# Optimization experiments

Hardware: AMD Instinct MI355X
Metric: run time of the kernel (lower is better)

## Reference

```python
import jax, jax.numpy as jnp
import numpy as np

D, H, HD, F, L, V, R = 4096, 32, 128, 11008, 2, 32002, 64
ALPHA = 16.0
B, S = 2, 1024
EPS = 1e-5


def setup_inputs() -> dict:
    key = jax.random.key(0)
    ks = jax.random.split(key, 24)
    n = lambda k, shape: (jax.random.normal(k, shape, jnp.float32) * 0.02)
    return {
        "input_ids": jax.random.randint(ks[0], (B, S), 0, V),
        "attention_mask": jnp.ones((B, S), jnp.int32),
        "embed": n(ks[1], (V, D)),
        "Wq": n(ks[2], (L, D, D)), "Wk": n(ks[3], (L, D, D)),
        "Wv": n(ks[4], (L, D, D)), "Wo": n(ks[5], (L, D, D)),
        "Aq": n(ks[6], (L, R, D)), "Bq": jnp.zeros((L, D, R), jnp.float32),
        "Ak": n(ks[7], (L, R, D)), "Bk": n(ks[8], (L, D, R)),
        "Av": n(ks[9], (L, R, D)), "Bv": n(ks[10], (L, D, R)),
        "Ao": n(ks[11], (L, R, D)), "Bo": n(ks[12], (L, D, R)),
        "Wgate": n(ks[13], (L, F, D)), "Wup": n(ks[14], (L, F, D)),
        "Wdown": n(ks[15], (L, D, F)),
        "attn_norm_w": jnp.ones((L, D), jnp.float32),
        "mlp_norm_w": jnp.ones((L, D), jnp.float32),
        "final_norm_w": jnp.ones((D,), jnp.float32),
        "cls_W": n(ks[16], (3, D)), "cls_b": jnp.zeros((3,), jnp.float32),
    }


def _rmsnorm(x, w):
    var = jnp.mean(jnp.square(x), axis=-1, keepdims=True)
    return (x * jax.lax.rsqrt(var + EPS)) * w


def _rope(seq_len):
    inv = 1.0 / (10000.0 ** (jnp.arange(0, HD, 2, dtype=jnp.float32) / HD))
    freqs = jnp.outer(jnp.arange(seq_len, dtype=jnp.float32), inv)  # [S, HD/2]
    emb = jnp.concatenate([freqs, freqs], -1)  # [S, HD]
    return jnp.cos(emb), jnp.sin(emb)


def _rot_half(x):
    h = x.shape[-1] // 2
    return jnp.concatenate([-x[..., h:], x[..., :h]], -1)


def _lora(h, W, A, Bm):
    # h @ W.T + (alpha/r) * (h @ A.T) @ B.T   (dropout inactive in eval)
    return h @ W.T + (h @ A.T) @ Bm.T * (ALPHA / R)


def reference(input_ids, attention_mask, embed, Wq, Wk, Wv, Wo,
              Aq, Bq, Ak, Bk, Av, Bv, Ao, Bo,
              Wgate, Wup, Wdown, attn_norm_w, mlp_norm_w, final_norm_w,
              cls_W, cls_b):
    b, s = input_ids.shape
    x = embed[input_ids]  # [B,S,D]
    cos, sin = _rope(s)  # [S,HD]
    causal = jnp.tril(jnp.ones((s, s), bool))
    mask = causal[None, None] & (attention_mask[:, None, None, :] > 0)
    bias = jnp.where(mask, 0.0, -1e9).astype(jnp.float32)  # [B,1,S,S]

    def heads(t):  # [B,S,D] -> [B,H,S,HD]
        return t.reshape(b, s, H, HD).transpose(0, 2, 1, 3)

    for l in range(L):
        h = _rmsnorm(x, attn_norm_w[l])
        q = heads(_lora(h, Wq[l], Aq[l], Bq[l]))
        k = heads(_lora(h, Wk[l], Ak[l], Bk[l]))
        v = heads(_lora(h, Wv[l], Av[l], Bv[l]))
        q = q * cos + _rot_half(q) * sin
        k = k * cos + _rot_half(k) * sin
        scores = jnp.einsum('bhqd,bhkd->bhqk', q, k) / np.sqrt(HD) + bias
        attn = jax.nn.softmax(scores, axis=-1)
        o = jnp.einsum('bhqk,bhkd->bhqd', attn, v)
        o = o.transpose(0, 2, 1, 3).reshape(b, s, D)
        x = x + _lora(o, Wo[l], Ao[l], Bo[l])
        h = _rmsnorm(x, mlp_norm_w[l])
        x = x + (jax.nn.silu(h @ Wgate[l].T) * (h @ Wup[l].T)) @ Wdown[l].T

    x = _rmsnorm(x, final_norm_w)
    cls = x[:, 0, :]  # [CLS] at position 0 (right padding)
    return cls @ cls_W.T + cls_b
```

## Files before the change

### kernel.cpp

```cpp
#include <hip/hip_runtime.h>
#include <cstdint>
#include <cstddef>

#define D_   4096
#define H_   32
#define HD_  128
#define F_   11008
#define L_   2
#define R_   64
#define BB   2
#define SS   1024
#define TOK  (BB*SS)
#define N3   12288
#define EPS_ 1e-5f

typedef __attribute__((ext_vector_type(8))) short          s16x8;
typedef __attribute__((ext_vector_type(4))) float          fx4;
typedef __attribute__((ext_vector_type(4))) unsigned short u16x4t;
typedef __attribute__((ext_vector_type(8))) unsigned short u16x8t;

__device__ __forceinline__ unsigned short f2bf(float f) {
  union { float f; unsigned u; } x; x.f = f;
  unsigned r = (x.u + 0x7FFFu + ((x.u >> 16) & 1u)) >> 16;
  return (unsigned short)r;
}
__device__ __forceinline__ float b2f(unsigned short h) {
  union { unsigned u; float f; } x; x.u = ((unsigned)h) << 16;
  return x.f;
}

__device__ __forceinline__ void xcd_remap(int nwg, int mt_cnt, int& mt, int& nt) {
  const int orig = blockIdx.x;
  const int q = nwg >> 3, r = nwg & 7;
  const int xcd = orig & 7, i = orig >> 3;
  const int wgid = (xcd < r ? xcd * (q + 1) : r * (q + 1) + (xcd - r) * q) + i;
  mt = wgid % mt_cnt;
  nt = wgid / mt_cnt;
}

__global__ void k_embed(const int* __restrict__ ids, const float* __restrict__ emb,
                        float* __restrict__ x) {
  const int tok = blockIdx.x, tid = threadIdx.x;
  const int id = ids[tok];
  const float* s = emb + (size_t)id * D_;
  float* d = x + (size_t)tok * D_;
#pragma unroll
  for (int i = 0; i < 4; ++i)
    *(fx4*)(d + i * 1024 + tid * 4) = *(const fx4*)(s + i * 1024 + tid * 4);
}

__global__ __launch_bounds__(256) void k_cvt(const float* __restrict__ src,
                                             unsigned short* __restrict__ dst, int n) {
  const int stride = gridDim.x * 256 * 8;
  for (int i = (blockIdx.x * 256 + threadIdx.x) * 8; i < n; i += stride) {
    fx4 a = *(const fx4*)(src + i);
    fx4 b = *(const fx4*)(src + i + 4);
    u16x8t p;
    p[0] = f2bf(a[0]); p[1] = f2bf(a[1]); p[2] = f2bf(a[2]); p[3] = f2bf(a[3]);
    p[4] = f2bf(b[0]); p[5] = f2bf(b[1]); p[6] = f2bf(b[2]); p[7] = f2bf(b[3]);
    *(u16x8t*)(dst + i) = p;
  }
}

__global__ __launch_bounds__(256) void k_rmsnorm(const float* __restrict__ x,
                                                 const float* __restrict__ w,
                                                 unsigned short* __restrict__ out) {
  const int row = blockIdx.x, tid = threadIdx.x;
  const float* xr = x + (size_t)row * D_;
  fx4 v[4];
  float ss = 0.f;
#pragma unroll
  for (int i = 0; i < 4; ++i) {
    v[i] = *(const fx4*)(xr + i * 1024 + tid * 4);
    ss += v[i][0]*v[i][0] + v[i][1]*v[i][1] + v[i][2]*v[i][2] + v[i][3]*v[i][3];
  }
#pragma unroll
  for (int off = 32; off > 0; off >>= 1) ss += __shfl_down(ss, off);
  __shared__ float red[4];
  if ((tid & 63) == 0) red[tid >> 6] = ss;
  __syncthreads();
  const float sc = rsqrtf((red[0] + red[1] + red[2] + red[3]) * (1.f / D_) + EPS_);
  unsigned short* orow = out + (size_t)row * D_;
#pragma unroll
  for (int i = 0; i < 4; ++i) {
    fx4 wv = *(const fx4*)(w + i * 1024 + tid * 4);
    u16x4t pk;
    pk.x = f2bf(v[i][0] * sc * wv[0]);
    pk.y = f2bf(v[i][1] * sc * wv[1]);
    pk.z = f2bf(v[i][2] * sc * wv[2]);
    pk.w = f2bf(v[i][3] * sc * wv[3]);
    *(u16x4t*)(orow + i * 1024 + tid * 4) = pk;
  }
}

template <int NFRAG>
__global__ __launch_bounds__(256, 2) void k_lmid(const unsigned short* __restrict__ Ain,
                                                 const float* __restrict__ P0,
                                                 const float* __restrict__ P1,
                                                 const float* __restrict__ P2,
                                                 float* __restrict__ part) {
  __shared__ unsigned short sA[64 * 64];
  __shared__ unsigned short sW[NFRAG * 16 * 72];
  const int tid = threadIdx.x, wave = tid >> 6, lane = tid & 63;
  const int l15 = lane & 15, l4 = lane >> 4;
  const int m0 = blockIdx.x * 64;
  const int kbase = blockIdx.y * 512;
  const int arow = tid >> 3;
  const int acol = (((tid & 7) ^ (arow & 7)) << 3);
  const int brow = tid >> 4;
  const int bcol = (tid & 15) << 2;
  const float* ptrs[3] = {P0, P1, P2};

  fx4 acc[NFRAG];
#pragma unroll
  for (int j = 0; j < NFRAG; ++j) acc[j] = (fx4){0.f, 0.f, 0.f, 0.f};

  for (int t = 0; t < 8; ++t) {
    const int kb = kbase + t * 64;
#pragma unroll
    for (int i = 0; i < 2; ++i) {
      const unsigned short* gp = Ain + (size_t)(m0 + i * 32 + arow) * 4096 + kb + acol;
      unsigned short* lp = sA + i * 2048 + wave * 512;
      __builtin_amdgcn_global_load_lds(
          (const __attribute__((address_space(1))) unsigned int*)gp,
          (__attribute__((address_space(3))) unsigned int*)lp, 16, 0, 0);
    }
#pragma unroll
    for (int j = 0; j < NFRAG; ++j) {
      const float* wp = ptrs[j >> 2] + (size_t)((j & 3) * 16 + brow) * 4096 + kb + bcol;
      fx4 v = *(const fx4*)wp;
      u16x4t pk;
      pk.x = f2bf(v[0]); pk.y = f2bf(v[1]); pk.z = f2bf(v[2]); pk.w = f2bf(v[3]);
      *(u16x4t*)&sW[(j * 16 + brow) * 72 + bcol] = pk;
    }
    __syncthreads();
#pragma unroll
    for (int ks = 0; ks < 2; ++ks) {
      const int row = wave * 16 + l15;
      const int cid = (((ks * 4) + l4) ^ (row & 7)) << 3;
      s16x8 af = *(const s16x8*)&sA[row * 64 + cid];
#pragma unroll
      for (int j = 0; j < NFRAG; ++j) {
        s16x8 bf = *(const s16x8*)&sW[(j * 16 + l15) * 72 + ks * 32 + (l4 << 3)];
        acc[j] = __builtin_amdgcn_mfma_f32_16x16x32_bf16(af, bf, acc[j], 0, 0, 0);
      }
    }
    __syncthreads();
  }
  const size_t base = (size_t)blockIdx.y * 2048 * (NFRAG * 16);
#pragma unroll
  for (int j = 0; j < NFRAG; ++j)
#pragma unroll
    for (int r = 0; r < 4; ++r)
      part[base + (size_t)(m0 + wave * 16 + l4 * 4 + r) * (NFRAG * 16) + j * 16 + l15] = acc[j][r];
}

__global__ void k_lmred(const float* __restrict__ part, unsigned short* __restrict__ outb, int ld) {
  const int idx = blockIdx.x * 256 + threadIdx.x;
  const int stride = 2048 * ld;
  float s = 0.f;
#pragma unroll
  for (int ks = 0; ks < 8; ++ks) s += part[(size_t)ks * stride + idx];
  outb[idx] = f2bf(0.25f * s);
}

template <int EPI, bool EXT>
__global__ __launch_bounds__(256, 4) void k_gemm(const unsigned short* __restrict__ A,
                                                 const unsigned short* __restrict__ Wb,
                                                 float* __restrict__ outF,
                                                 unsigned short* __restrict__ outB,
                                                 const float* __restrict__ auxF,
                                                 const unsigned short* __restrict__ Aext,
                                                 int ldaE,
                                                 const unsigned short* __restrict__ Wext,
                                                 int M, int N, int K, int nwg) {
  __shared__ unsigned short sA[128 * 64];
  __shared__ unsigned short sB[128 * 64];
  const int tid = threadIdx.x;
  const int wave = tid >> 6, lane = tid & 63;
  int mt, nt;
  xcd_remap(nwg, M >> 7, mt, nt);
  const int m0 = mt * 128, n0 = nt * 128;
  const int wr = wave >> 1, wc = wave & 1;
  const int l15 = lane & 15, l4 = lane >> 4;

  fx4 acc[4][4];
#pragma unroll
  for (int i = 0; i < 4; ++i)
#pragma unroll
    for (int j = 0; j < 4; ++j) acc[i][j] = (fx4){0.f, 0.f, 0.f, 0.f};

  const int nsteps = K >> 6;
  const int arow = tid >> 3;
  const int acol = (((tid & 7) ^ (arow & 7)) << 3);

  for (int t = 0; t < nsteps; ++t) {
    const int kb = t << 6;
#pragma unroll
    for (int i = 0; i < 4; ++i) {
      const unsigned short* gp = A + (size_t)(m0 + i * 32 + arow) * K + kb + acol;
      unsigned short* lp = sA + i * 2048 + wave * 512;
      __builtin_amdgcn_global_load_lds(
          (const __attribute__((address_space(1))) unsigned int*)gp,
          (__attribute__((address_space(3))) unsigned int*)lp, 16, 0, 0);
    }
#pragma unroll
    for (int i = 0; i < 4; ++i) {
      const unsigned short* gp = Wb + (size_t)(n0 + i * 32 + arow) * K + kb + acol;
      unsigned short* lp = sB + i * 2048 + wave * 512;
      __builtin_amdgcn_global_load_lds(
          (const __attribute__((address_space(1))) unsigned int*)gp,
          (__attribute__((address_space(3))) unsigned int*)lp, 16, 0, 0);
    }
    __syncthreads();
#pragma unroll
    for (int ks = 0; ks < 2; ++ks) {
      s16x8 af[4], bfr[4];
#pragma unroll
      for (int i = 0; i < 4; ++i) {
        int row = wr * 64 + i * 16 + l15;
        int cid = (((ks * 4) + l4) ^ (row & 7)) << 3;
        af[i] = *(const s16x8*)&sA[row * 64 + cid];
      }
#pragma unroll
      for (int j = 0; j < 4; ++j) {
        int row = wc * 64 + j * 16 + l15;
        int cid = (((ks * 4) + l4) ^ (row & 7)) << 3;
        bfr[j] = *(const s16x8*)&sB[row * 64 + cid];
      }
#pragma unroll
      for (int i = 0; i < 4; ++i)
#pragma unroll
        for (int j = 0; j < 4; ++j)
          acc[i][j] = __builtin_amdgcn_mfma_f32_16x16x32_bf16(af[i], bfr[j], acc[i][j], 0, 0, 0);
    }
    __syncthreads();
  }

  if constexpr (EXT) {
    const int third = n0 >> 12;
    const unsigned short* Ae = Aext + third * 64;
    const unsigned short* We = Wext + (size_t)n0 * 64;
#pragma unroll
    for (int i = 0; i < 4; ++i) {
      const unsigned short* gp = Ae + (size_t)(m0 + i * 32 + arow) * ldaE + acol;
      unsigned short* lp = sA + i * 2048 + wave * 512;
      __builtin_amdgcn_global_load_lds(
          (const __attribute__((address_space(1))) unsigned int*)gp,
          (__attribute__((address_space(3))) unsigned int*)lp, 16, 0, 0);
    }
#pragma unroll
    for (int i = 0; i < 4; ++i) {
      const unsigned short* gp = We + (size_t)(i * 32 + arow) * 64 + acol;
      unsigned short* lp = sB + i * 2048 + wave * 512;
      __builtin_amdgcn_global_load_lds(
          (const __attribute__((address_space(1))) unsigned int*)gp,
          (__attribute__((address_space(3))) unsigned int*)lp, 16, 0, 0);
    }
    __syncthreads();
#pragma unroll
    for (int ks = 0; ks < 2; ++ks) {
      s16x8 af[4], bfr[4];
#pragma unroll
      for (int i = 0; i < 4; ++i) {
        int row = wr * 64 + i * 16 + l15;
        int cid = (((ks * 4) + l4) ^ (row & 7)) << 3;
        af[i] = *(const s16x8*)&sA[row * 64 + cid];
      }
#pragma unroll
      for (int j = 0; j < 4; ++j) {
        int row = wc * 64 + j * 16 + l15;
        int cid = (((ks * 4) + l4) ^ (row & 7)) << 3;
        bfr[j] = *(const s16x8*)&sB[row * 64 + cid];
      }
#pragma unroll
      for (int i = 0; i < 4; ++i)
#pragma unroll
        for (int j = 0; j < 4; ++j)
          acc[i][j] = __builtin_amdgcn_mfma_f32_16x16x32_bf16(af[i], bfr[j], acc[i][j], 0, 0, 0);
    }
  }

  const int r0 = m0 + wr * 64 + (l4 << 2);
  const int c0 = n0 + wc * 64 + l15;
#pragma unroll
  for (int i = 0; i < 4; ++i)
#pragma unroll
    for (int j = 0; j < 4; ++j)
#pragma unroll
      for (int r = 0; r < 4; ++r) {
        size_t idx = (size_t)(r0 + i * 16 + r) * N + (c0 + j * 16);
        float v = acc[i][j][r];
        if (EPI == 2) outF[idx] = v + auxF[idx];
        else          outB[idx] = f2bf(v);
      }
}

__global__ __launch_bounds__(256, 2) void k_gemm_gu2(const unsigned short* __restrict__ A,
                                                     const unsigned short* __restrict__ Wg,
                                                     const unsigned short* __restrict__ Wu,
                                                     unsigned short* __restrict__ outB,
                                                     int M, int N, int K, int nwg) {
  __shared__ unsigned short sA[128 * 64];
  __shared__ unsigned short sG[128 * 64];
  __shared__ unsigned short sU[128 * 64];
  const int tid = threadIdx.x;
  const int wave = tid >> 6, lane = tid & 63;
  int mt, nt;
  xcd_remap(nwg, M >> 7, mt, nt);
  const int m0 = mt * 128, n0 = nt * 128;
  const int wr = wave >> 1, wc = wave & 1;
  const int l15 = lane & 15, l4 = lane >> 4;

  fx4 accg[4][4], accu[4][4];
#pragma unroll
  for (int i = 0; i < 4; ++i)
#pragma unroll
    for (int j = 0; j < 4; ++j) {
      accg[i][j] = (fx4){0.f, 0.f, 0.f, 0.f};
      accu[i][j] = (fx4){0.f, 0.f, 0.f, 0.f};
    }

  const int nsteps = K >> 6;
  const int arow = tid >> 3;
  const int acol = (((tid & 7) ^ (arow & 7)) << 3);

  for (int t = 0; t < nsteps; ++t) {
    const int kb = t << 6;
#pragma unroll
    for (int i = 0; i < 4; ++i) {
      const unsigned short* gp = A + (size_t)(m0 + i * 32 + arow) * K + kb + acol;
      unsigned short* lp = sA + i * 2048 + wave * 512;
      __builtin_amdgcn_global_load_lds(
          (const __attribute__((address_space(1))) unsigned int*)gp,
          (__attribute__((address_space(3))) unsigned int*)lp, 16, 0, 0);
    }
#pragma unroll
    for (int i = 0; i < 4; ++i) {
      const unsigned short* gp = Wg + (size_t)(n0 + i * 32 + arow) * K + kb + acol;
      unsigned short* lp = sG + i * 2048 + wave * 512;
      __builtin_amdgcn_global_load_lds(
          (const __attribute__((address_space(1))) unsigned int*)gp,
          (__attribute__((address_space(3))) unsigned int*)lp, 16, 0, 0);
    }
#pragma unroll
    for (int i = 0; i < 4; ++i) {
      const unsigned short* gp = Wu + (size_t)(n0 + i * 32 + arow) * K + kb + acol;
      unsigned short* lp = sU + i * 2048 + wave * 512;
      __builtin_amdgcn_global_load_lds(
          (const __attribute__((address_space(1))) unsigned int*)gp,
          (__attribute__((address_space(3))) unsigned int*)lp, 16, 0, 0);
    }
    __syncthreads();
#pragma unroll
    for (int ks = 0; ks < 2; ++ks) {
      s16x8 af[4], bg[4], bu[4];
#pragma unroll
      for (int i = 0; i < 4; ++i) {
        int row = wr * 64 + i * 16 + l15;
        int cid = (((ks * 4) + l4) ^ (row & 7)) << 3;
        af[i] = *(const s16x8*)&sA[row * 64 + cid];
      }
#pragma unroll
      for (int j = 0; j < 4; ++j) {
        int row = wc * 64 + j * 16 + l15;
        int cid = (((ks * 4) + l4) ^ (row & 7)) << 3;
        bg[j] = *(const s16x8*)&sG[row * 64 + cid];
        bu[j] = *(const s16x8*)&sU[row * 64 + cid];
      }
#pragma unroll
      for (int i = 0; i < 4; ++i)
#pragma unroll
        for (int j = 0; j < 4; ++j) {
          accg[i][j] = __builtin_amdgcn_mfma_f32_16x16x32_bf16(af[i], bg[j], accg[i][j], 0, 0, 0);
          accu[i][j] = __builtin_amdgcn_mfma_f32_16x16x32_bf16(af[i], bu[j], accu[i][j], 0, 0, 0);
        }
    }
    __syncthreads();
  }

  const int r0 = m0 + wr * 64 + (l4 << 2);
  const int c0 = n0 + wc * 64 + l15;
#pragma unroll
  for (int i = 0; i < 4; ++i)
#pragma unroll
    for (int j = 0; j < 4; ++j)
#pragma unroll
      for (int r = 0; r < 4; ++r) {
        size_t idx = (size_t)(r0 + i * 16 + r) * N + (c0 + j * 16);
        float g = accg[i][j][r];
        outB[idx] = f2bf(accu[i][j][r] * g / (1.f + __expf(-g)));
      }
}

__global__ void k_ropetab(float* __restrict__ cosT, float* __restrict__ sinT) {
  int idx = blockIdx.x * 256 + threadIdx.x;
  int s = idx >> 6, d = idx & 63;
  float inv = powf(10000.f, -(float)d * (1.f / 64.f));
  float f = (float)s * inv;
  cosT[idx] = cosf(f);
  sinT[idx] = sinf(f);
}

__global__ __launch_bounds__(256) void k_kvprep(const unsigned short* __restrict__ P3,
                                                const float* __restrict__ cosT,
                                                const float* __restrict__ sinT,
                                                unsigned short* __restrict__ kb,
                                                unsigned short* __restrict__ vb) {
  __shared__ unsigned short sT[128 * 72];
  const int tid = threadIdx.x;
  const int bh = blockIdx.y, b = bh >> 5, h = bh & 31;
  const int k0 = blockIdx.x * 64;
  {
    int row = tid >> 2, part = tid & 3;
    int ksr = k0 + row;
    const unsigned short* kp = P3 + (size_t)(b * SS + ksr) * N3 + 4096 + h * HD_;
    const float* cr = cosT + ksr * 64;
    const float* sr = sinT + ksr * 64;
    unsigned short* kd = kb + ((size_t)bh * SS + ksr) * HD_;
#pragma unroll
    for (int g = 0; g < 2; ++g) {
      int d0 = part * 16 + g * 8;
      u16x8t klo = *(const u16x8t*)(kp + d0);
      u16x8t khi = *(const u16x8t*)(kp + d0 + 64);
      u16x8t wlo, whi;
#pragma unroll
      for (int j = 0; j < 8; ++j) {
        float lo = b2f(klo[j]), hi = b2f(khi[j]);
        float c = cr[d0 + j], s = sr[d0 + j];
        wlo[j] = f2bf(lo * c - hi * s);
        whi[j] = f2bf(hi * c + lo * s);
      }
      *(u16x8t*)(kd + d0)      = wlo;
      *(u16x8t*)(kd + d0 + 64) = whi;
    }
  }
  {
#pragma unroll
    for (int it = 0; it < 8; ++it) {
      int key = it * 8 + (tid >> 5), hd0 = (tid & 31) * 4;
      u16x4t v = *(const u16x4t*)(P3 + (size_t)(b * SS + k0 + key) * N3 + 8192 + h * HD_ + hd0);
      sT[(hd0 + 0) * 72 + key] = v.x;
      sT[(hd0 + 1) * 72 + key] = v.y;
      sT[(hd0 + 2) * 72 + key] = v.z;
      sT[(hd0 + 3) * 72 + key] = v.w;
    }
    __syncthreads();
    int hd = tid >> 1, half = tid & 1;
    unsigned short* vd = vb + ((size_t)bh * HD_ + hd) * SS + k0 + half * 32;
    const unsigned short* ssrc = sT + hd * 72 + half * 32;
#pragma unroll
    for (int j = 0; j < 4; ++j)
      *(u16x8t*)(vd + j * 8) = *(const u16x8t*)(ssrc + j * 8);
  }
}

__global__ __launch_bounds__(256, 3) void k_attn(const unsigned short* __restrict__ P3,
                                                 const unsigned short* __restrict__ kb,
                                                 const unsigned short* __restrict__ vb,
                                                 const float* __restrict__ cosT,
                                                 const float* __restrict__ sinT,
                                                 const int* __restrict__ am,
                                                 unsigned short* __restrict__ O) {
  __shared__ unsigned short sK[64 * 128];
  __shared__ unsigned short sV[128 * 64];
  __shared__ unsigned short sP[4 * 16 * 72];
  const int tid = threadIdx.x, wave = tid >> 6, lane = tid & 63;
  const int bh = blockIdx.y, b = bh >> 5, h = bh & 31;
  const int qt = (int)gridDim.x - 1 - blockIdx.x;
  const float scale = 0.08838834764831845f;
  const int l15 = lane & 15, l4 = lane >> 4;

  const int qs = qt * 64 + wave * 16 + l15;
  s16x8 qf[4];
  {
    const unsigned short* qp = P3 + (size_t)(b * SS + qs) * N3 + h * HD_;
    const float* cr = cosT + qs * 64;
    const float* sr = sinT + qs * 64;
#pragma unroll
    for (int ks = 0; ks < 2; ++ks) {
      int dlo = ks * 32 + l4 * 8;
      u16x8t qlo = *(const u16x8t*)(qp + dlo);
      u16x8t qhi = *(const u16x8t*)(qp + dlo + 64);
      u16x8t plo, phi;
#pragma unroll
      for (int j = 0; j < 8; ++j) {
        float lo = b2f(qlo[j]), hi = b2f(qhi[j]);
        float c = cr[dlo + j], s = sr[dlo + j];
        plo[j] = f2bf(lo * c - hi * s);
        phi[j] = f2bf(hi * c + lo * s);
      }
      qf[ks]     = *(s16x8*)&plo;
      qf[ks + 2] = *(s16x8*)&phi;
    }
  }

  const int krow_l = lane >> 4, kg = lane & 15;
  const int vrow_l = lane >> 3, vg = lane & 7;

  fx4 oacc[8];
#pragma unroll
  for (int nf = 0; nf < 8; ++nf) oacc[nf] = (fx4){0.f, 0.f, 0.f, 0.f};
  float mrun[4] = {-1e30f, -1e30f, -1e30f, -1e30f};
  float lrun[4] = {0.f, 0.f, 0.f, 0.f};

  const int ntiles = qt + 1;
  for (int kt = 0; kt < ntiles; ++kt) {
    const int k0 = kt * 64;
    __syncthreads();
#pragma unroll
    for (int i = 0; i < 4; ++i) {
      int row = (i * 4 + wave) * 4 + krow_l;
      const unsigned short* gp = kb + ((size_t)bh * SS + k0 + row) * HD_ + ((kg ^ (row & 7)) << 3);
      unsigned short* lp = sK + (i * 4 + wave) * 512;
      __builtin_amdgcn_global_load_lds(
          (const __attribute__((address_space(1))) unsigned int*)gp,
          (__attribute__((address_space(3))) unsigned int*)lp, 16, 0, 0);
    }
#pragma unroll
    for (int i = 0; i < 4; ++i) {
      int row = (i * 4 + wave) * 8 + vrow_l;
      const unsigned short* gp = vb + ((size_t)bh * HD_ + row) * SS + k0 + ((vg ^ (row & 7)) << 3);
      unsigned short* lp = sV + (i * 4 + wave) * 512;
      __builtin_amdgcn_global_load_lds(
          (const __attribute__((address_space(1))) unsigned int*)gp,
          (__attribute__((address_space(3))) unsigned int*)lp, 16, 0, 0);
    }
    __syncthreads();
    if (k0 <= qt * 64 + wave * 16 + 15) {
      fx4 sfr[4];
#pragma unroll
      for (int kf = 0; kf < 4; ++kf) sfr[kf] = (fx4){0.f, 0.f, 0.f, 0.f};
#pragma unroll
      for (int kf = 0; kf < 4; ++kf) {
        int row = kf * 16 + l15;
#pragma unroll
        for (int ks = 0; ks < 4; ++ks) {
          int cid = ((ks * 4 + l4) ^ (row & 7)) << 3;
          s16x8 kfr = *(const s16x8*)&sK[row * 128 + cid];
          sfr[kf] = __builtin_amdgcn_mfma_f32_16x16x32_bf16(qf[ks], kfr, sfr[kf], 0, 0, 0);
        }
      }
      float p[16], corr[4];
#pragma unroll
      for (int r = 0; r < 4; ++r) {
        int qr = qt * 64 + wave * 16 + l4 * 4 + r;
        float mx = -1e30f;
#pragma unroll
        for (int kf = 0; kf < 4; ++kf) {
          int key = k0 + kf * 16 + l15;
          float bb = (key <= qr && am[b * SS + key] != 0) ? 0.f : -1e9f;
          p[kf * 4 + r] = sfr[kf][r] * scale + bb;
          mx = fmaxf(mx, p[kf * 4 + r]);
        }
        mx = fmaxf(mx, __shfl_xor(mx, 1));
        mx = fmaxf(mx, __shfl_xor(mx, 2));
        mx = fmaxf(mx, __shfl_xor(mx, 4));
        mx = fmaxf(mx, __shfl_xor(mx, 8));
        float mn = fmaxf(mrun[r], mx);
        corr[r] = __expf(mrun[r] - mn);
        mrun[r] = mn;
        float rs = 0.f;
#pragma unroll
        for (int kf = 0; kf < 4; ++kf) {
          p[kf * 4 + r] = __expf(p[kf * 4 + r] - mn);
          rs += p[kf * 4 + r];
        }
        rs += __shfl_xor(rs, 1);
        rs += __shfl_xor(rs, 2);
        rs += __shfl_xor(rs, 4);
        rs += __shfl_xor(rs, 8);
        lrun[r] = lrun[r] * corr[r] + rs;
      }
#pragma unroll
      for (int nf = 0; nf < 8; ++nf) {
        oacc[nf][0] *= corr[0];
        oacc[nf][1] *= corr[1];
        oacc[nf][2] *= corr[2];
        oacc[nf][3] *= corr[3];
      }
      unsigned short* pp = sP + wave * (16 * 72);
#pragma unroll
      for (int r = 0; r < 4; ++r) {
        int row = l4 * 4 + r;
#pragma unroll
        for (int kf = 0; kf < 4; ++kf)
          pp[row * 72 + kf * 16 + l15] = f2bf(p[kf * 4 + r]);
      }
      s16x8 pa0 = *(const s16x8*)&pp[l15 * 72 + l4 * 8];
      s16x8 pa1 = *(const s16x8*)&pp[l15 * 72 + 32 + l4 * 8];
#pragma unroll
      for (int nf = 0; nf < 8; ++nf) {
        int row = nf * 16 + l15;
        int c0s = ((0 * 4 + l4) ^ (row & 7)) << 3;
        int c1s = ((1 * 4 + l4) ^ (row & 7)) << 3;
        s16x8 v0 = *(const s16x8*)&sV[row * 64 + c0s];
        s16x8 v1 = *(const s16x8*)&sV[row * 64 + c1s];
        oacc[nf] = __builtin_amdgcn_mfma_f32_16x16x32_bf16(pa0, v0, oacc[nf], 0, 0, 0);
        oacc[nf] = __builtin_amdgcn_mfma_f32_16x16x32_bf16(pa1, v1, oacc[nf], 0, 0, 0);
      }
    }
  }
  const size_t obase = (size_t)b * SS * D_ + h * HD_;
#pragma unroll
  for (int nf = 0; nf < 8; ++nf)
#pragma unroll
    for (int r = 0; r < 4; ++r) {
      int qr = qt * 64 + wave * 16 + l4 * 4 + r;
      O[obase + (size_t)qr * D_ + nf * 16 + l15] = f2bf(oacc[nf][r] / lrun[r]);
    }
}

__global__ __launch_bounds__(256) void k_final(const float* __restrict__ xf,
                                               const float* __restrict__ fw,
                                               const float* __restrict__ cW,
                                               const float* __restrict__ cb,
                                               float* __restrict__ out) {
  const int b = blockIdx.x, tid = threadIdx.x;
  const float* xr = xf + (size_t)b * SS * D_;
  __shared__ float red[4];
  fx4 v[4];
  float ss = 0.f;
#pragma unroll
  for (int i = 0; i < 4; ++i) {
    v[i] = *(const fx4*)(xr + i * 1024 + tid * 4);
    ss += v[i][0]*v[i][0] + v[i][1]*v[i][1] + v[i][2]*v[i][2] + v[i][3]*v[i][3];
  }
#pragma unroll
  for (int off = 32; off > 0; off >>= 1) ss += __shfl_down(ss, off);
  if ((tid & 63) == 0) red[tid >> 6] = ss;
  __syncthreads();
  const float sc = rsqrtf((red[0] + red[1] + red[2] + red[3]) * (1.f / D_) + EPS_);
  for (int c = 0; c < 3; ++c) {
    float d = 0.f;
#pragma unroll
    for (int i = 0; i < 4; ++i) {
      fx4 fv = *(const fx4*)(fw + i * 1024 + tid * 4);
      fx4 cw = *(const fx4*)(cW + (size_t)c * D_ + i * 1024 + tid * 4);
#pragma unroll
      for (int j = 0; j < 4; ++j) d += v[i][j] * sc * fv[j] * cw[j];
    }
#pragma unroll
    for (int off = 32; off > 0; off >>= 1) d += __shfl_down(d, off);
    __syncthreads();
    if ((tid & 63) == 0) red[tid >> 6] = d;
    __syncthreads();
    if (tid == 0) out[b * 3 + c] = red[0] + red[1] + red[2] + red[3] + cb[c];
  }
}

extern "C" void kernel_launch(void* const* d_in, const int* in_sizes, int n_in,
                              void* d_out, int out_size, void* d_ws, size_t ws_size,
                              hipStream_t stream) {
  const int*   ids = (const int*)d_in[0];
  const int*   am  = (const int*)d_in[1];
  const float* emb = (const float*)d_in[2];
  const float* Wq  = (const float*)d_in[3];
  const float* Wk  = (const float*)d_in[4];
  const float* Wv  = (const float*)d_in[5];
  const float* Wo  = (const float*)d_in[6];
  const float* Aq  = (const float*)d_in[7];
  const float* Bq  = (const float*)d_in[8];
  const float* Ak  = (const float*)d_in[9];
  const float* Bk  = (const float*)d_in[10];
  const float* Av  = (const float*)d_in[11];
  const float* Bv  = (const float*)d_in[12];
  const float* Ao  = (const float*)d_in[13];
  const float* Bo  = (const float*)d_in[14];
  const float* Wg  = (const float*)d_in[15];
  const float* Wu  = (const float*)d_in[16];
  const float* Wd  = (const float*)d_in[17];
  const float* anw = (const float*)d_in[18];
  const float* mnw = (const float*)d_in[19];
  const float* fnw = (const float*)d_in[20];
  const float* cW  = (const float*)d_in[21];
  const float* cb  = (const float*)d_in[22];
  float* out = (float*)d_out;

  char* w = (char*)d_ws;
  float* xf = (float*)w;                     w += (size_t)TOK * D_ * 4;
  unsigned short* P3 = (unsigned short*)w;   w += (size_t)TOK * N3 * 2;
  unsigned short* gact = (unsigned short*)w; w += (size_t)TOK * F_ * 2;
  unsigned short* hb = (unsigned short*)w;   w += (size_t)TOK * D_ * 2;
  unsigned short* ob = (unsigned short*)w;   w += (size_t)TOK * D_ * 2;
  unsigned short* kbuf = (unsigned short*)w; w += (size_t)TOK * D_ * 2;
  unsigned short* vbuf = (unsigned short*)w; w += (size_t)TOK * D_ * 2;
  unsigned short* Wm3 = (unsigned short*)w;  w += (size_t)3 * D_ * D_ * 2;
  unsigned short* Wgu = (unsigned short*)w;  w += (size_t)2 * F_ * D_ * 2;
  unsigned short* Bx3 = (unsigned short*)w;  w += (size_t)3 * D_ * R_ * 2;
  unsigned short* BxO = (unsigned short*)w;  w += (size_t)D_ * R_ * 2;
  unsigned short* lm3 = (unsigned short*)w;  w += (size_t)TOK * 192 * 2;
  unsigned short* lmo = (unsigned short*)w;  w += (size_t)TOK * 64 * 2;
  float* lm3p = (float*)w;                   w += (size_t)8 * TOK * 192 * 4;
  float* lmop = (float*)w;                   w += (size_t)8 * TOK * 64 * 4;
  float* cosT = (float*)w;                   w += (size_t)SS * 64 * 4;
  float* sinT = (float*)w;                   w += (size_t)SS * 64 * 4;
  if ((size_t)(w - (char*)d_ws) > ws_size) return;

  k_ropetab<<<256, 256, 0, stream>>>(cosT, sinT);
  k_embed<<<TOK, 256, 0, stream>>>(ids, emb, xf);

  const int nwgQKV = (N3 / 128) * (TOK / 128);
  const int nwgProj = (D_ / 128) * (TOK / 128);
  const int nwgMlp = (F_ / 128) * (TOK / 128);
  dim3 gAttn(SS / 64, BB * H_);
  dim3 gPrep(SS / 64, BB * H_);
  dim3 gLmid(TOK / 64, 8);
  const int CVT_BLK = 2048;

  for (int l = 0; l < L_; ++l) {
    const size_t oDD = (size_t)l * D_ * D_;
    const size_t oRD = (size_t)l * R_ * D_;
    const size_t oDR = (size_t)l * D_ * R_;
    const size_t oFD = (size_t)l * F_ * D_;

    k_rmsnorm<<<TOK, 256, 0, stream>>>(xf, anw + (size_t)l * D_, hb);
    k_cvt<<<CVT_BLK, 256, 0, stream>>>(Wq + oDD, Wm3, D_ * D_);
    k_cvt<<<CVT_BLK, 256, 0, stream>>>(Wk + oDD, Wm3 + (size_t)D_ * D_, D_ * D_);
    k_cvt<<<CVT_BLK, 256, 0, stream>>>(Wv + oDD, Wm3 + (size_t)2 * D_ * D_, D_ * D_);
    k_cvt<<<128, 256, 0, stream>>>(Bq + oDR, Bx3, D_ * R_);
    k_cvt<<<128, 256, 0, stream>>>(Bk + oDR, Bx3 + (size_t)D_ * R_, D_ * R_);
    k_cvt<<<128, 256, 0, stream>>>(Bv + oDR, Bx3 + (size_t)2 * D_ * R_, D_ * R_);
    k_lmid<12><<<gLmid, 256, 0, stream>>>(hb, Aq + oRD, Ak + oRD, Av + oRD, lm3p);
    k_lmred<<<TOK * 192 / 256, 256, 0, stream>>>(lm3p, lm3, 192);
    k_gemm<5, true><<<nwgQKV, 256, 0, stream>>>(hb, Wm3, nullptr, P3, nullptr,
                                                lm3, 192, Bx3, TOK, N3, D_, nwgQKV);
    k_kvprep<<<gPrep, 256, 0, stream>>>(P3, cosT, sinT, kbuf, vbuf);
    k_attn<<<gAttn, 256, 0, stream>>>(P3, kbuf, vbuf, cosT, sinT, am, ob);
    k_cvt<<<CVT_BLK, 256, 0, stream>>>(Wo + oDD, Wm3, D_ * D_);
    k_cvt<<<128, 256, 0, stream>>>(Bo + oDR, BxO, D_ * R_);
    k_lmid<4><<<gLmid, 256, 0, stream>>>(ob, Ao + oRD, Ao + oRD, Ao + oRD, lmop);
    k_lmred<<<TOK * 64 / 256, 256, 0, stream>>>(lmop, lmo, 64);
    k_gemm<2, true><<<nwgProj, 256, 0, stream>>>(ob, Wm3, xf, nullptr, xf,
                                                 lmo, 64, BxO, TOK, D_, D_, nwgProj);
    k_rmsnorm<<<TOK, 256, 0, stream>>>(xf, mnw + (size_t)l * D_, hb);
    k_cvt<<<CVT_BLK, 256, 0, stream>>>(Wg + oFD, Wgu, F_ * D_);
    k_cvt<<<CVT_BLK, 256, 0, stream>>>(Wu + oFD, Wgu + (size_t)F_ * D_, F_ * D_);
    k_gemm_gu2<<<nwgMlp, 256, 0, stream>>>(hb, Wgu, Wgu + (size_t)F_ * D_, gact, TOK, F_, D_, nwgMlp);
    k_cvt<<<CVT_BLK, 256, 0, stream>>>(Wd + oFD, Wgu, D_ * F_);
    k_gemm<2, false><<<nwgProj, 256, 0, stream>>>(gact, Wgu, xf, nullptr, xf,
                                                  nullptr, 0, nullptr, TOK, D_, F_, nwgProj);
  }

  k_final<<<BB, 256, 0, stream>>>(xf, fnw, cW, cb, out);
  (void)in_sizes; (void)n_in; (void)out_size;
}
```

Baseline: 2.664 ms.

## Widen QKV GEMM tile to 128x256 and batch weight conversions into multi-source launches

Adds a new QKV projection GEMM kernel in which each workgroup computes a 128x256 output tile with two accumulator sets. Each A tile loaded into LDS is reused across twice as many output columns, and the LoRA extension term is folded in the same way. Separate fp32-to-bf16 weight conversion launches are merged into single launches with a y-dimension that selects the source. The wider tile roughly doubles accumulator registers and LDS per workgroup, which can reduce occupancy, and it halves the number of workgroups.

```diff
diff --git a/kernel.cpp b/kernel.cpp
--- a/kernel.cpp
+++ b/kernel.cpp
@@ -49,8 +49,12 @@
     *(fx4*)(d + i * 1024 + tid * 4) = *(const fx4*)(s + i * 1024 + tid * 4);
 }
 
-__global__ __launch_bounds__(256) void k_cvt(const float* __restrict__ src,
-                                             unsigned short* __restrict__ dst, int n) {
+__global__ __launch_bounds__(256) void k_cvtN(const float* __restrict__ s0,
+                                              const float* __restrict__ s1,
+                                              const float* __restrict__ s2,
+                                              unsigned short* __restrict__ dst, int n) {
+  const float* src = blockIdx.y == 0 ? s0 : (blockIdx.y == 1 ? s1 : s2);
+  unsigned short* d = dst + (size_t)blockIdx.y * n;
   const int stride = gridDim.x * 256 * 8;
   for (int i = (blockIdx.x * 256 + threadIdx.x) * 8; i < n; i += stride) {
     fx4 a = *(const fx4*)(src + i);
@@ -58,7 +62,7 @@
     u16x8t p;
     p[0] = f2bf(a[0]); p[1] = f2bf(a[1]); p[2] = f2bf(a[2]); p[3] = f2bf(a[3]);
     p[4] = f2bf(b[0]); p[5] = f2bf(b[1]); p[6] = f2bf(b[2]); p[7] = f2bf(b[3]);
-    *(u16x8t*)(dst + i) = p;
+    *(u16x8t*)(d + i) = p;
   }
 }
 
@@ -293,6 +297,168 @@
         float v = acc[i][j][r];
         if (EPI == 2) outF[idx] = v + auxF[idx];
         else          outB[idx] = f2bf(v);
+      }
+}
+
+template <int EPI, bool EXT>
+__global__ __launch_bounds__(256, 2) void k_gemm2(const unsigned short* __restrict__ A,
+                                                  const unsigned short* __restrict__ Wb,
+                                                  float* __restrict__ outF,
+                                                  unsigned short* __restrict__ outB,
+                                                  const float* __restrict__ auxF,
+                                                  const unsigned short* __restrict__ Aext,
+                                                  int ldaE,
+                                                  const unsigned short* __restrict__ Wext,
+                                                  int M, int N, int K, int nwg) {
+  __shared__ unsigned short sA[128 * 64];
+  __shared__ unsigned short sB0[128 * 64];
+  __shared__ unsigned short sB1[128 * 64];
+  const int tid = threadIdx.x;
+  const int wave = tid >> 6, lane = tid & 63;
+  int mt, nt;
+  xcd_remap(nwg, M >> 7, mt, nt);
+  const int m0 = mt * 128, n0 = nt * 256;
+  const int wr = wave >> 1, wc = wave & 1;
+  const int l15 = lane & 15, l4 = lane >> 4;
+
+  fx4 acc0[4][4], acc1[4][4];
+#pragma unroll
+  for (int i = 0; i < 4; ++i)
+#pragma unroll
+    for (int j = 0; j < 4; ++j) {
+      acc0[i][j] = (fx4){0.f, 0.f, 0.f, 0.f};
+      acc1[i][j] = (fx4){0.f, 0.f, 0.f, 0.f};
+    }
+
+  const int nsteps = K >> 6;
+  const int arow = tid >> 3;
+  const int acol = (((tid & 7) ^ (arow & 7)) << 3);
+
+  for (int t = 0; t < nsteps; ++t) {
+    const int kb = t << 6;
+#pragma unroll
+    for (int i = 0; i < 4; ++i) {
+      const unsigned short* gp = A + (size_t)(m0 + i * 32 + arow) * K + kb + acol;
+      unsigned short* lp = sA + i * 2048 + wave * 512;
+      __builtin_amdgcn_global_load_lds(
+          (const __attribute__((address_space(1))) unsigned int*)gp,
+          (__attribute__((address_space(3))) unsigned int*)lp, 16, 0, 0);
+    }
+#pragma unroll
+    for (int i = 0; i < 4; ++i) {
+      const unsigned short* gp = Wb + (size_t)(n0 + i * 32 + arow) * K + kb + acol;
+      unsigned short* lp = sB0 + i * 2048 + wave * 512;
+      __builtin_amdgcn_global_load_lds(
+          (const __attribute__((address_space(1))) unsigned int*)gp,
+          (__attribute__((address_space(3))) unsigned int*)lp, 16, 0, 0);
+    }
+#pragma unroll
+    for (int i = 0; i < 4; ++i) {
+      const unsigned short* gp = Wb + (size_t)(n0 + 128 + i * 32 + arow) * K + kb + acol;
+      unsigned short* lp = sB1 + i * 2048 + wave * 512;
+      __builtin_amdgcn_global_load_lds(
+          (const __attribute__((address_space(1))) unsigned int*)gp,
+          (__attribute__((address_space(3))) unsigned int*)lp, 16, 0, 0);
+    }
+    __syncthreads();
+#pragma unroll
+    for (int ks = 0; ks < 2; ++ks) {
+      s16x8 af[4], b0[4], b1[4];
+#pragma unroll
+      for (int i = 0; i < 4; ++i) {
+        int row = wr * 64 + i * 16 + l15;
+        int cid = (((ks * 4) + l4) ^ (row & 7)) << 3;
+        af[i] = *(const s16x8*)&sA[row * 64 + cid];
+      }
+#pragma unroll
+      for (int j = 0; j < 4; ++j) {
+        int row = wc * 64 + j * 16 + l15;
+        int cid = (((ks * 4) + l4) ^ (row & 7)) << 3;
+        b0[j] = *(const s16x8*)&sB0[row * 64 + cid];
+        b1[j] = *(const s16x8*)&sB1[row * 64 + cid];
+      }
+#pragma unroll
+      for (int i = 0; i < 4; ++i)
+#pragma unroll
+        for (int j = 0; j < 4; ++j) {
+          acc0[i][j] = __builtin_amdgcn_mfma_f32_16x16x32_bf16(af[i], b0[j], acc0[i][j], 0, 0, 0);
+          acc1[i][j] = __builtin_amdgcn_mfma_f32_16x16x32_bf16(af[i], b1[j], acc1[i][j], 0, 0, 0);
+        }
+    }
+    __syncthreads();
+  }
+
+  if constexpr (EXT) {
+    const int third = n0 >> 12;
+    const unsigned short* Ae = Aext + third * 64;
+#pragma unroll
+    for (int i = 0; i < 4; ++i) {
+      const unsigned short* gp = Ae + (size_t)(m0 + i * 32 + arow) * ldaE + acol;
+      unsigned short* lp = sA + i * 2048 + wave * 512;
+      __builtin_amdgcn_global_load_lds(
+          (const __attribute__((address_space(1))) unsigned int*)gp,
+          (__attribute__((address_space(3))) unsigned int*)lp, 16, 0, 0);
+    }
+#pragma unroll
+    for (int i = 0; i < 4; ++i) {
+      const unsigned short* gp = Wext + (size_t)(n0 + i * 32 + arow) * 64 + acol;
+      unsigned short* lp = sB0 + i * 2048 + wave * 512;
+      __builtin_amdgcn_global_load_lds(
+          (const __attribute__((address_space(1))) unsigned int*)gp,
+          (__attribute__((address_space(3))) unsigned int*)lp, 16, 0, 0);
+    }
+#pragma unroll
+    for (int i = 0; i < 4; ++i) {
+      const unsigned short* gp = Wext + (size_t)(n0 + 128 + i * 32 + arow) * 64 + acol;
+      unsigned short* lp = sB1 + i * 2048 + wave * 512;
+      __builtin_amdgcn_global_load_lds(
+          (const __attribute__((address_space(1))) unsigned int*)gp,
+          (__attribute__((address_space(3))) unsigned int*)lp, 16, 0, 0);
+    }
+    __syncthreads();
+#pragma unroll
+    for (int ks = 0; ks < 2; ++ks) {
+      s16x8 af[4], b0[4], b1[4];
+#pragma unroll
+      for (int i = 0; i < 4; ++i) {
+        int row = wr * 64 + i * 16 + l15;
+        int cid = (((ks * 4) + l4) ^ (row & 7)) << 3;
+        af[i] = *(const s16x8*)&sA[row * 64 + cid];
+      }
+#pragma unroll
+      for (int j = 0; j < 4; ++j) {
+        int row = wc * 64 + j * 16 + l15;
+        int cid = (((ks * 4) + l4) ^ (row & 7)) << 3;
+        b0[j] = *(const s16x8*)&sB0[row * 64 + cid];
+        b1[j] = *(const s16x8*)&sB1[row * 64 + cid];
+      }
+#pragma unroll
+      for (int i = 0; i < 4; ++i)
+#pragma unroll
+        for (int j = 0; j < 4; ++j) {
+          acc0[i][j] = __builtin_amdgcn_mfma_f32_16x16x32_bf16(af[i], b0[j], acc0[i][j], 0, 0, 0);
+          acc1[i][j] = __builtin_amdgcn_mfma_f32_16x16x32_bf16(af[i], b1[j], acc1[i][j], 0, 0, 0);
+        }
+    }
+  }
+
+  const int r0 = m0 + wr * 64 + (l4 << 2);
+  const int c0 = n0 + wc * 64 + l15;
+#pragma unroll
+  for (int i = 0; i < 4; ++i)
+#pragma unroll
+    for (int j = 0; j < 4; ++j)
+#pragma unroll
+      for (int r = 0; r < 4; ++r) {
+        size_t idx0 = (size_t)(r0 + i * 16 + r) * N + (c0 + j * 16);
+        size_t idx1 = idx0 + 128;
+        if (EPI == 2) {
+          outF[idx0] = acc0[i][j][r] + auxF[idx0];
+          outF[idx1] = acc1[i][j][r] + auxF[idx1];
+        } else {
+          outB[idx0] = f2bf(acc0[i][j][r]);
+          outB[idx1] = f2bf(acc1[i][j][r]);
+        }
       }
 }
 
@@ -700,7 +866,7 @@
   k_ropetab<<<256, 256, 0, stream>>>(cosT, sinT);
   k_embed<<<TOK, 256, 0, stream>>>(ids, emb, xf);
 
-  const int nwgQKV = (N3 / 128) * (TOK / 128);
+  const int nwgQKV2 = (TOK / 128) * (N3 / 256);
   const int nwgProj = (D_ / 128) * (TOK / 128);
   const int nwgMlp = (F_ / 128) * (TOK / 128);
   dim3 gAttn(SS / 64, BB * H_);
@@ -715,29 +881,24 @@
     const size_t oFD = (size_t)l * F_ * D_;
 
     k_rmsnorm<<<TOK, 256, 0, stream>>>(xf, anw + (size_t)l * D_, hb);
-    k_cvt<<<CVT_BLK, 256, 0, stream>>>(Wq + oDD, Wm3, D_ * D_);
-    k_cvt<<<CVT_BLK, 256, 0, stream>>>(Wk + oDD, Wm3 + (size_t)D_ * D_, D_ * D_);
-    k_cvt<<<CVT_BLK, 256, 0, stream>>>(Wv + oDD, Wm3 + (size_t)2 * D_ * D_, D_ * D_);
-    k_cvt<<<128, 256, 0, stream>>>(Bq + oDR, Bx3, D_ * R_);
-    k_cvt<<<128, 256, 0, stream>>>(Bk + oDR, Bx3 + (size_t)D_ * R_, D_ * R_);
-    k_cvt<<<128, 256, 0, stream>>>(Bv + oDR, Bx3 + (size_t)2 * D_ * R_, D_ * R_);
+    k_cvtN<<<dim3(CVT_BLK, 3), 256, 0, stream>>>(Wq + oDD, Wk + oDD, Wv + oDD, Wm3, D_ * D_);
+    k_cvtN<<<dim3(128, 3), 256, 0, stream>>>(Bq + oDR, Bk + oDR, Bv + oDR, Bx3, D_ * R_);
     k_lmid<12><<<gLmid, 256, 0, stream>>>(hb, Aq + oRD, Ak + oRD, Av + oRD, lm3p);
     k_lmred<<<TOK * 192 / 256, 256, 0, stream>>>(lm3p, lm3, 192);
-    k_gemm<5, true><<<nwgQKV, 256, 0, stream>>>(hb, Wm3, nullptr, P3, nullptr,
-                                                lm3, 192, Bx3, TOK, N3, D_, nwgQKV);
+    k_gemm2<5, true><<<nwgQKV2, 256, 0, stream>>>(hb, Wm3, nullptr, P3, nullptr,
+                                                  lm3, 192, Bx3, TOK, N3, D_, nwgQKV2);
     k_kvprep<<<gPrep, 256, 0, stream>>>(P3, cosT, sinT, kbuf, vbuf);
     k_attn<<<gAttn, 256, 0, stream>>>(P3, kbuf, vbuf, cosT, sinT, am, ob);
-    k_cvt<<<CVT_BLK, 256, 0, stream>>>(Wo + oDD, Wm3, D_ * D_);
-    k_cvt<<<128, 256, 0, stream>>>(Bo + oDR, BxO, D_ * R_);
+    k_cvtN<<<dim3(CVT_BLK, 1), 256, 0, stream>>>(Wo + oDD, nullptr, nullptr, Wm3, D_ * D_);
+    k_cvtN<<<dim3(128, 1), 256, 0, stream>>>(Bo + oDR, nullptr, nullptr, BxO, D_ * R_);
     k_lmid<4><<<gLmid, 256, 0, stream>>>(ob, Ao + oRD, Ao + oRD, Ao + oRD, lmop);
     k_lmred<<<TOK * 64 / 256, 256, 0, stream>>>(lmop, lmo, 64);
     k_gemm<2, true><<<nwgProj, 256, 0, stream>>>(ob, Wm3, xf, nullptr, xf,
                                                  lmo, 64, BxO, TOK, D_, D_, nwgProj);
     k_rmsnorm<<<TOK, 256, 0, stream>>>(xf, mnw + (size_t)l * D_, hb);
-    k_cvt<<<CVT_BLK, 256, 0, stream>>>(Wg + oFD, Wgu, F_ * D_);
-    k_cvt<<<CVT_BLK, 256, 0, stream>>>(Wu + oFD, Wgu + (size_t)F_ * D_, F_ * D_);
+    k_cvtN<<<dim3(CVT_BLK, 2), 256, 0, stream>>>(Wg + oFD, Wu + oFD, nullptr, Wgu, F_ * D_);
     k_gemm_gu2<<<nwgMlp, 256, 0, stream>>>(hb, Wgu, Wgu + (size_t)F_ * D_, gact, TOK, F_, D_, nwgMlp);
-    k_cvt<<<CVT_BLK, 256, 0, stream>>>(Wd + oFD, Wgu, D_ * F_);
+    k_cvtN<<<dim3(CVT_BLK, 1), 256, 0, stream>>>(Wd + oFD, nullptr, nullptr, Wgu, D_ * F_);
     k_gemm<2, false><<<nwgProj, 256, 0, stream>>>(gact, Wgu, xf, nullptr, xf,
                                                   nullptr, 0, nullptr, TOK, D_, F_, nwgProj);
   }
```

Result: slower. 2.725 ms (+2.3%).
